# Kernel tuning notes

Measured on AMD Instinct MI355X. Metric: run time of the kernel, lower is better.

## Reference

```python
import jax, jax.numpy as jnp
import numpy as np

N_NODES = 50000
N_REL = 16
N_BASIS = 8
D_IN = 64
D_HID = 64
N_CLASS = 16
N_EDGES = 800000


def setup_inputs() -> dict:
    key = jax.random.key(0)
    ks = jax.random.split(key, 9)
    x = jax.random.normal(ks[0], (N_NODES, D_IN), dtype=jnp.float32)
    edge_index = jax.random.randint(ks[1], (2, N_EDGES), 0, N_NODES, dtype=jnp.int64)
    edge_type = jax.random.randint(ks[2], (N_EDGES,), 0, N_REL, dtype=jnp.int64)
    s1 = 1.0 / np.sqrt(D_IN)
    s2 = 1.0 / np.sqrt(D_HID)
    # layer 1: basis decomposition W_r = sum_b coeffs[r,b] * bases[b]
    bases1 = jax.random.normal(ks[3], (N_BASIS, D_IN, D_HID), dtype=jnp.float32) * s1
    coeffs1 = jax.random.normal(ks[4], (N_REL, N_BASIS), dtype=jnp.float32)
    self1 = jax.random.normal(ks[5], (D_IN, D_HID), dtype=jnp.float32) * s1
    # layer 2
    bases2 = jax.random.normal(ks[6], (N_BASIS, D_HID, N_CLASS), dtype=jnp.float32) * s2
    coeffs2 = jax.random.normal(ks[7], (N_REL, N_BASIS), dtype=jnp.float32)
    self2 = jax.random.normal(ks[8], (D_HID, N_CLASS), dtype=jnp.float32) * s2
    return {"x": x, "bases1": bases1, "coeffs1": coeffs1, "self1": self1,
            "bases2": bases2, "coeffs2": coeffs2, "self2": self2,
            "edge_index": edge_index, "edge_type": edge_type}


def _rgcn_layer(h, bases, coeffs, self_w, src, seg_id, inv_c):
    # normalized messages gathered from source nodes: [E, d]
    msg = h[src] * inv_c[:, None]
    # fused per-(relation, target-node) segment reduce -> [R, N, d]
    agg = jax.ops.segment_sum(msg, seg_id, num_segments=N_REL * N_NODES)
    agg = agg.reshape(N_REL, N_NODES, -1)
    # per-relation weights from basis decomposition: [R, d_in, d_out]
    w_rel = jnp.einsum('rb,bio->rio', coeffs, bases)
    return jnp.einsum('rni,rio->no', agg, w_rel) + h @ self_w


def reference(x, bases1, coeffs1, self1, bases2, coeffs2, self2, edge_index, edge_type):
    src, dst = edge_index[0], edge_index[1]
    # normalization constants: per-relation in-degree of each target node
    counts = jnp.zeros((N_REL, N_NODES), dtype=jnp.float32).at[edge_type, dst].add(1.0)
    inv_c = 1.0 / jnp.maximum(counts[edge_type, dst], 1.0)  # [E]
    seg_id = edge_type * N_NODES + dst  # combined (relation, node) segment key
    h = jax.nn.relu(_rgcn_layer(x, bases1, coeffs1, self1, src, seg_id, inv_c))
    logits = _rgcn_layer(h, bases2, coeffs2, self2, src, seg_id, inv_c)
    return logits
```

## Files before the change

kernel.cpp:

```cpp
#include <hip/hip_runtime.h>

#define N_NODES 50000
#define N_REL 16
#define N_BASIS 8
#define N_EDGES 800000
#define G1_BLOCKS 782
#define SC_BLOCKS 3125
#define WREL_BLOCKS 340
#define ZERO_BLOCKS 49
#define CAP 64

typedef short s8v __attribute__((ext_vector_type(8)));
typedef float f4v __attribute__((ext_vector_type(4)));

__device__ inline unsigned short f2bf(float f) {
    union { float f; unsigned u; } v; v.f = f;
    unsigned r = (v.u + 0x7FFFu + ((v.u >> 16) & 1u)) >> 16;
    return (unsigned short)r;
}
__device__ inline float bf2f(unsigned short b) {
    union { unsigned u; float f; } v; v.u = ((unsigned)b) << 16;
    return v.f;
}
__device__ __forceinline__ void acc8(float* a, float inv, int4 p) {
    a[0] += inv * __int_as_float((int)((unsigned)p.x << 16));
    a[1] += inv * __int_as_float(p.x & (int)0xFFFF0000u);
    a[2] += inv * __int_as_float((int)((unsigned)p.y << 16));
    a[3] += inv * __int_as_float(p.y & (int)0xFFFF0000u);
    a[4] += inv * __int_as_float((int)((unsigned)p.z << 16));
    a[5] += inv * __int_as_float(p.z & (int)0xFFFF0000u);
    a[6] += inv * __int_as_float((int)((unsigned)p.w << 16));
    a[7] += inv * __int_as_float(p.w & (int)0xFFFF0000u);
}

__global__ __launch_bounds__(256) void k_pre(const float* __restrict__ b1, const float* __restrict__ c1,
                                             const float* __restrict__ s1f,
                                             const float* __restrict__ b2, const float* __restrict__ c2,
                                             const float* __restrict__ s2f,
                                             unsigned short* __restrict__ w1T,
                                             unsigned short* __restrict__ w2T,
                                             int* __restrict__ cursor) {
    int bid = blockIdx.x;
    if (bid >= WREL_BLOCKS) {
        int i = (bid - WREL_BLOCKS) * 256 + threadIdx.x;
        if (i < 12504) ((int4*)cursor)[i] = make_int4(0, 0, 0, 0);
        return;
    }
    int idx = bid * 256 + threadIdx.x;
    if (idx < 17 * 4096) {
        int r = idx >> 12, o = (idx >> 6) & 63, k = idx & 63;
        float acc = 0.f;
        if (r < 16) {
            #pragma unroll
            for (int b = 0; b < N_BASIS; b++) acc += c1[r * N_BASIS + b] * b1[b * 4096 + k * 64 + o];
        } else {
            acc = s1f[k * 64 + o];
        }
        w1T[idx] = f2bf(acc);
    } else {
        int idx2 = idx - 17 * 4096;
        if (idx2 < 17 * 1024) {
            int r = idx2 >> 10, o = (idx2 >> 6) & 15, k = idx2 & 63;
            float acc = 0.f;
            if (r < 16) {
                #pragma unroll
                for (int b = 0; b < N_BASIS; b++) acc += c2[r * N_BASIS + b] * b2[b * 1024 + k * 16 + o];
            } else {
                acc = s2f[k * 16 + o];
            }
            w2T[idx2] = f2bf(acc);
        }
    }
}

__device__ __forceinline__ void gemm1_tile(int tile, int tid,
                                           const float* __restrict__ x,
                                           const unsigned short* __restrict__ w1T,
                                           unsigned short* __restrict__ t1,
                                           unsigned short* __restrict__ h,
                                           unsigned short* wbuf,
                                           unsigned short* ou) {
    int wv = tid >> 6, lane = tid & 63;
    int m = lane & 15, q = lane >> 4;
    int nb = tile * 64 + wv * 16;
    bool active = (nb < N_NODES);
    int n = active ? (nb + m) : 0;

    const float* xr = x + (size_t)n * 64 + q * 8;
    float4 x0a = *(const float4*)(xr);
    float4 x0b = *(const float4*)(xr + 4);
    float4 x1a = *(const float4*)(xr + 32);
    float4 x1b = *(const float4*)(xr + 36);
    s8v b0, b1;
    b0[0] = f2bf(x0a.x); b0[1] = f2bf(x0a.y); b0[2] = f2bf(x0a.z); b0[3] = f2bf(x0a.w);
    b0[4] = f2bf(x0b.x); b0[5] = f2bf(x0b.y); b0[6] = f2bf(x0b.z); b0[7] = f2bf(x0b.w);
    b1[0] = f2bf(x1a.x); b1[1] = f2bf(x1a.y); b1[2] = f2bf(x1a.z); b1[3] = f2bf(x1a.w);
    b1[4] = f2bf(x1b.x); b1[5] = f2bf(x1b.y); b1[6] = f2bf(x1b.z); b1[7] = f2bf(x1b.w);

    int c0 = tid, c1 = tid + 256;
    int p0s = (c0 >> 3) * 64 + (((c0 & 7) ^ ((c0 >> 3) & 7)) << 3);
    int p1s = (c1 >> 3) * 64 + (((c1 & 7) ^ ((c1 >> 3) & 7)) << 3);

    {
        const int4* src = (const int4*)w1T;
        int4 v0 = src[c0], v1 = src[c1];
        *(int4*)&wbuf[p0s] = v0;
        *(int4*)&wbuf[p1s] = v1;
    }
    __syncthreads();

    for (int w = 0; w < 17; w++) {
        int cur = w & 1;
        if (w < 16) {
            const int4* src = (const int4*)w1T + (w + 1) * 512;
            int4 v0 = src[c0], v1 = src[c1];
            *(int4*)&wbuf[(cur ^ 1) * 4096 + p0s] = v0;
            *(int4*)&wbuf[(cur ^ 1) * 4096 + p1s] = v1;
        }
        #pragma unroll
        for (int ct = 0; ct < 4; ct++) {
            int ro = ct * 16 + m;
            int pa = q ^ (ro & 7);
            int pb = (4 + q) ^ (ro & 7);
            s8v A0 = *(const s8v*)&wbuf[cur * 4096 + ro * 64 + pa * 8];
            s8v A1 = *(const s8v*)&wbuf[cur * 4096 + ro * 64 + pb * 8];
            f4v acc = (f4v){0.f, 0.f, 0.f, 0.f};
            acc = __builtin_amdgcn_mfma_f32_16x16x32_bf16(A0, b0, acc, 0, 0, 0);
            acc = __builtin_amdgcn_mfma_f32_16x16x32_bf16(A1, b1, acc, 0, 0, 0);
            ushort4 o4;
            o4.x = f2bf(acc[0]); o4.y = f2bf(acc[1]); o4.z = f2bf(acc[2]); o4.w = f2bf(acc[3]);
            int g = ct * 2 + (q >> 1);
            int pg = g ^ (m & 7);
            *(ushort4*)&ou[wv * 1024 + m * 64 + pg * 8 + (q & 1) * 4] = o4;
        }
        if (active) {
            int r1 = lane >> 3, g1 = lane & 7;
            int pg1 = g1 ^ (r1 & 7);
            int4 d0 = *(const int4*)&ou[wv * 1024 + r1 * 64 + pg1 * 8];
            int4 d1 = *(const int4*)&ou[wv * 1024 + (r1 + 8) * 64 + pg1 * 8];
            unsigned short* base = (w < 16) ? (t1 + ((size_t)w * N_NODES + nb) * 64)
                                            : (h + (size_t)nb * 64);
            *(int4*)(base + lane * 8) = d0;
            *(int4*)(base + 512 + lane * 8) = d1;
        }
        __syncthreads();
    }
}

__global__ __launch_bounds__(256) void k_fused1(const float* __restrict__ x,
                                                const unsigned short* __restrict__ w1T,
                                                unsigned short* __restrict__ t1,
                                                unsigned short* __restrict__ h,
                                                const int* __restrict__ ei,
                                                const int* __restrict__ et,
                                                int* __restrict__ cursor,
                                                int* __restrict__ sed) {
    __shared__ __align__(16) unsigned short wbuf[2 * 4096];
    __shared__ __align__(16) unsigned short ou[4 * 1024];
    if (blockIdx.x >= G1_BLOCKS) {
        int e = (blockIdx.x - G1_BLOCKS) * 256 + threadIdx.x;
        if (e < N_EDGES) {
            int src = ei[e];
            int dst = ei[N_EDGES + e];
            int t = et[e];
            int pos = atomicAdd(&cursor[dst], 1);
            if (pos < CAP) sed[dst * CAP + pos] = (t << 16) | src;
        }
        return;
    }
    gemm1_tile(blockIdx.x, threadIdx.x, x, w1T, t1, h, wbuf, ou);
}

__global__ __launch_bounds__(256) void k_aggt(const int* __restrict__ cursor,
                                              const int* __restrict__ sed,
                                              const unsigned short* __restrict__ t1,
                                              const unsigned short* __restrict__ h,
                                              const unsigned short* __restrict__ w2T,
                                              unsigned short* __restrict__ t2,
                                              float* __restrict__ out) {
    __shared__ int hist[16][16];
    __shared__ __align__(16) unsigned short htile[16][72];
    int tid = threadIdx.x;
    int nb = blockIdx.x * 16;
    int j = tid >> 4;
    int sub = tid & 15;
    int n = nb + j;
    int deg = cursor[n];
    deg = deg < CAP ? deg : CAP;
    const int* bucket = sed + n * CAP;

    hist[j][sub] = 0;
    for (int i = sub; i < deg; i += 16)
        atomicAdd(&hist[j][bucket[i] >> 16], 1);

    int slot = sub >> 3;
    int d8 = sub & 7;
    float a[8];
    #pragma unroll
    for (int k = 0; k < 8; k++) a[k] = 0.f;
    for (int i = slot; i < deg; i += 4) {
        int e0 = bucket[i];
        bool has1 = (i + 2) < deg;
        int e1 = has1 ? bucket[i + 2] : e0;
        int t0 = e0 >> 16, s0 = e0 & 0xFFFF;
        int t1i = e1 >> 16, s1 = e1 & 0xFFFF;
        float inv0 = 1.0f / (float)hist[j][t0];
        float inv1 = has1 ? (1.0f / (float)hist[j][t1i]) : 0.f;
        int4 p0 = *(const int4*)(t1 + ((size_t)(t0 * N_NODES + s0)) * 64 + d8 * 8);
        int4 p1 = *(const int4*)(t1 + ((size_t)(t1i * N_NODES + s1)) * 64 + d8 * 8);
        acc8(a, inv0, p0);
        acc8(a, inv1, p1);
    }
    #pragma unroll
    for (int k = 0; k < 8; k++) a[k] += __shfl_xor(a[k], 8, 64);
    if (slot == 0) {
        int4 hs = *(const int4*)(h + (size_t)n * 64 + d8 * 8);
        acc8(a, 1.0f, hs);
        ushort4 lo, hi;
        lo.x = f2bf(a[0] > 0.f ? a[0] : 0.f);
        lo.y = f2bf(a[1] > 0.f ? a[1] : 0.f);
        lo.z = f2bf(a[2] > 0.f ? a[2] : 0.f);
        lo.w = f2bf(a[3] > 0.f ? a[3] : 0.f);
        hi.x = f2bf(a[4] > 0.f ? a[4] : 0.f);
        hi.y = f2bf(a[5] > 0.f ? a[5] : 0.f);
        hi.z = f2bf(a[6] > 0.f ? a[6] : 0.f);
        hi.w = f2bf(a[7] > 0.f ? a[7] : 0.f);
        *(ushort4*)&htile[j][d8 * 8] = lo;
        *(ushort4*)&htile[j][d8 * 8 + 4] = hi;
    }
    __syncthreads();

    int wv = tid >> 6, lane = tid & 63;
    int m = lane & 15, q = lane >> 4;
    int nn = nb + m;
    s8v b0 = *(const s8v*)&htile[m][q * 8];
    s8v b1 = *(const s8v*)&htile[m][32 + q * 8];
    const unsigned short* wp = w2T + m * 64 + q * 8;

    #pragma unroll
    for (int j5 = 0; j5 < 4; j5++) {
        int w = wv * 4 + j5;
        s8v A0 = *(const s8v*)(wp + (w << 10));
        s8v A1 = *(const s8v*)(wp + (w << 10) + 32);
        f4v acc = (f4v){0.f, 0.f, 0.f, 0.f};
        acc = __builtin_amdgcn_mfma_f32_16x16x32_bf16(A0, b0, acc, 0, 0, 0);
        acc = __builtin_amdgcn_mfma_f32_16x16x32_bf16(A1, b1, acc, 0, 0, 0);
        ushort4 o;
        o.x = f2bf(acc[0]); o.y = f2bf(acc[1]); o.z = f2bf(acc[2]); o.w = f2bf(acc[3]);
        *(ushort4*)(t2 + ((size_t)w * N_NODES + nn) * 16 + q * 4) = o;
    }
    if (wv == 0) {
        s8v A0 = *(const s8v*)(wp + (16 << 10));
        s8v A1 = *(const s8v*)(wp + (16 << 10) + 32);
        f4v acc = (f4v){0.f, 0.f, 0.f, 0.f};
        acc = __builtin_amdgcn_mfma_f32_16x16x32_bf16(A0, b0, acc, 0, 0, 0);
        acc = __builtin_amdgcn_mfma_f32_16x16x32_bf16(A1, b1, acc, 0, 0, 0);
        *(float4*)(out + (size_t)nn * 16 + q * 4) = make_float4(acc[0], acc[1], acc[2], acc[3]);
    }
}

__global__ __launch_bounds__(256) void k_agg2(const int* __restrict__ cursor,
                                              const int* __restrict__ sed,
                                              const unsigned short* __restrict__ t2,
                                              float* __restrict__ out) {
    __shared__ int hist[16][16];
    int tid = threadIdx.x;
    int j = tid >> 4;
    int sub = tid & 15;
    int n = blockIdx.x * 16 + j;
    int deg = cursor[n];
    deg = deg < CAP ? deg : CAP;
    const int* bucket = sed + n * CAP;

    hist[j][sub] = 0;
    for (int i = sub; i < deg; i += 16)
        atomicAdd(&hist[j][bucket[i] >> 16], 1);

    int slot = sub >> 1;
    int d2 = sub & 1;
    float a[8];
    #pragma unroll
    for (int k = 0; k < 8; k++) a[k] = 0.f;
    for (int i = slot; i < deg; i += 16) {
        int e0 = bucket[i];
        bool has1 = (i + 8) < deg;
        int e1 = has1 ? bucket[i + 8] : e0;
        int t0 = e0 >> 16, s0 = e0 & 0xFFFF;
        int t1i = e1 >> 16, s1 = e1 & 0xFFFF;
        float inv0 = 1.0f / (float)hist[j][t0];
        float inv1 = has1 ? (1.0f / (float)hist[j][t1i]) : 0.f;
        int4 p0 = *(const int4*)(t2 + ((size_t)(t0 * N_NODES + s0)) * 16 + d2 * 8);
        int4 p1 = *(const int4*)(t2 + ((size_t)(t1i * N_NODES + s1)) * 16 + d2 * 8);
        acc8(a, inv0, p0);
        acc8(a, inv1, p1);
    }
    #pragma unroll
    for (int k = 0; k < 8; k++) {
        a[k] += __shfl_xor(a[k], 2, 64);
        a[k] += __shfl_xor(a[k], 4, 64);
        a[k] += __shfl_xor(a[k], 8, 64);
    }
    if (slot == 0) {
        float* p = out + (size_t)n * 16 + d2 * 8;
        float4 c0 = *(const float4*)p;
        float4 c1 = *(const float4*)(p + 4);
        c0.x += a[0]; c0.y += a[1]; c0.z += a[2]; c0.w += a[3];
        c1.x += a[4]; c1.y += a[5]; c1.z += a[6]; c1.w += a[7];
        *(float4*)p = c0;
        *(float4*)(p + 4) = c1;
    }
}

extern "C" void kernel_launch(void* const* d_in, const int* in_sizes, int n_in,
                              void* d_out, int out_size, void* d_ws, size_t ws_size,
                              hipStream_t stream) {
    const float* x      = (const float*)d_in[0];
    const float* bases1 = (const float*)d_in[1];
    const float* coeffs1= (const float*)d_in[2];
    const float* self1  = (const float*)d_in[3];
    const float* bases2 = (const float*)d_in[4];
    const float* coeffs2= (const float*)d_in[5];
    const float* self2  = (const float*)d_in[6];
    const int*   ei     = (const int*)d_in[7];
    const int*   et     = (const int*)d_in[8];
    float* out = (float*)d_out;

    char* ws = (char*)d_ws;
    int*            cursor = (int*)(ws + 0);
    unsigned short* w1T    = (unsigned short*)(ws + 200064);
    unsigned short* w2T    = (unsigned short*)(ws + 339328);
    int*            sed    = (int*)(ws + 374144);
    unsigned short* h      = (unsigned short*)(ws + 13174144);
    unsigned short* t1     = (unsigned short*)(ws + 19574144);
    unsigned short* t2     = (unsigned short*)(ws + 121974144);

    k_pre<<<WREL_BLOCKS + ZERO_BLOCKS, 256, 0, stream>>>(
        bases1, coeffs1, self1, bases2, coeffs2, self2, w1T, w2T, cursor);
    k_fused1<<<G1_BLOCKS + SC_BLOCKS, 256, 0, stream>>>(x, w1T, t1, h, ei, et, cursor, sed);
    k_aggt<<<SC_BLOCKS, 256, 0, stream>>>(cursor, sed, t1, h, w2T, t2, out);
    k_agg2<<<SC_BLOCKS, 256, 0, stream>>>(cursor, sed, t2, out);
}
```

Measured before the change: 183.4 us.

## Aggregate raw features per relation before transforming instead of pre-transforming all nodes

Drops the old order of transforming every node by all 17 relation weight matrices and then gathering. Each node now first gathers and mean-averages its neighbours' bf16 features per relation in shared memory, after sorting its edges by relation with a histogram and prefix sum. It then applies the relation weights with MFMA over the 16 per-relation aggregates plus the self term. This removes the large t1/t2 intermediates (16×N×64 bf16 for layer one) and their write/read traffic. In exchange the per-node bucket sort costs shared-memory atomics and syncs, the per-relation gather loops are serialized, the second layer's matmul runs on only one wave, and x gets a separate bf16 conversion pass.

Result: slower. 327.0 us (+78.3%).

```diff
diff --git a/kernel.cpp b/kernel.cpp
--- a/kernel.cpp
+++ b/kernel.cpp
@@ -4,11 +4,13 @@
 #define N_REL 16
 #define N_BASIS 8
 #define N_EDGES 800000
-#define G1_BLOCKS 782
-#define SC_BLOCKS 3125
+#define CAP 64
+
 #define WREL_BLOCKS 340
 #define ZERO_BLOCKS 49
-#define CAP 64
+#define XBF_BLOCKS 1563
+#define SC_BLOCKS 3125
+#define AGG_BLOCKS 3125
 
 typedef short s8v __attribute__((ext_vector_type(8)));
 typedef float f4v __attribute__((ext_vector_type(4)));
@@ -18,29 +20,38 @@
     unsigned r = (v.u + 0x7FFFu + ((v.u >> 16) & 1u)) >> 16;
     return (unsigned short)r;
 }
-__device__ inline float bf2f(unsigned short b) {
-    union { unsigned u; float f; } v; v.u = ((unsigned)b) << 16;
-    return v.f;
-}
-__device__ __forceinline__ void acc8(float* a, float inv, int4 p) {
-    a[0] += inv * __int_as_float((int)((unsigned)p.x << 16));
-    a[1] += inv * __int_as_float(p.x & (int)0xFFFF0000u);
-    a[2] += inv * __int_as_float((int)((unsigned)p.y << 16));
-    a[3] += inv * __int_as_float(p.y & (int)0xFFFF0000u);
-    a[4] += inv * __int_as_float((int)((unsigned)p.z << 16));
-    a[5] += inv * __int_as_float(p.z & (int)0xFFFF0000u);
-    a[6] += inv * __int_as_float((int)((unsigned)p.w << 16));
-    a[7] += inv * __int_as_float(p.w & (int)0xFFFF0000u);
-}
-
-__global__ __launch_bounds__(256) void k_pre(const float* __restrict__ b1, const float* __restrict__ c1,
+
+__device__ __forceinline__ void acc4(float* a, int2 p) {
+    a[0] += __int_as_float((int)((unsigned)p.x << 16));
+    a[1] += __int_as_float(p.x & (int)0xFFFF0000u);
+    a[2] += __int_as_float((int)((unsigned)p.y << 16));
+    a[3] += __int_as_float(p.y & (int)0xFFFF0000u);
+}
+
+__global__ __launch_bounds__(256) void k_pre(const float* __restrict__ x,
+                                             const float* __restrict__ b1, const float* __restrict__ c1,
                                              const float* __restrict__ s1f,
                                              const float* __restrict__ b2, const float* __restrict__ c2,
                                              const float* __restrict__ s2f,
                                              unsigned short* __restrict__ w1T,
                                              unsigned short* __restrict__ w2T,
+                                             unsigned short* __restrict__ xbf,
                                              int* __restrict__ cursor) {
     int bid = blockIdx.x;
+    if (bid >= WREL_BLOCKS + ZERO_BLOCKS) {
+        int i = (bid - WREL_BLOCKS - ZERO_BLOCKS) * 256 + threadIdx.x;
+        if (i < 400000) {
+            const float4* xs = (const float4*)x + (size_t)i * 2;
+            float4 v0 = xs[0], v1 = xs[1];
+            int4 w;
+            w.x = (int)(((unsigned)f2bf(v0.y) << 16) | f2bf(v0.x));
+            w.y = (int)(((unsigned)f2bf(v0.w) << 16) | f2bf(v0.z));
+            w.z = (int)(((unsigned)f2bf(v1.y) << 16) | f2bf(v1.x));
+            w.w = (int)(((unsigned)f2bf(v1.w) << 16) | f2bf(v1.z));
+            *(int4*)(xbf + (size_t)i * 8) = w;
+        }
+        return;
+    }
     if (bid >= WREL_BLOCKS) {
         int i = (bid - WREL_BLOCKS) * 256 + threadIdx.x;
         if (i < 12504) ((int4*)cursor)[i] = make_int4(0, 0, 0, 0);
@@ -73,242 +84,162 @@
     }
 }
 
-__device__ __forceinline__ void gemm1_tile(int tile, int tid,
-                                           const float* __restrict__ x,
-                                           const unsigned short* __restrict__ w1T,
-                                           unsigned short* __restrict__ t1,
-                                           unsigned short* __restrict__ h,
-                                           unsigned short* wbuf,
-                                           unsigned short* ou) {
-    int wv = tid >> 6, lane = tid & 63;
-    int m = lane & 15, q = lane >> 4;
-    int nb = tile * 64 + wv * 16;
-    bool active = (nb < N_NODES);
-    int n = active ? (nb + m) : 0;
-
-    const float* xr = x + (size_t)n * 64 + q * 8;
-    float4 x0a = *(const float4*)(xr);
-    float4 x0b = *(const float4*)(xr + 4);
-    float4 x1a = *(const float4*)(xr + 32);
-    float4 x1b = *(const float4*)(xr + 36);
-    s8v b0, b1;
-    b0[0] = f2bf(x0a.x); b0[1] = f2bf(x0a.y); b0[2] = f2bf(x0a.z); b0[3] = f2bf(x0a.w);
-    b0[4] = f2bf(x0b.x); b0[5] = f2bf(x0b.y); b0[6] = f2bf(x0b.z); b0[7] = f2bf(x0b.w);
-    b1[0] = f2bf(x1a.x); b1[1] = f2bf(x1a.y); b1[2] = f2bf(x1a.z); b1[3] = f2bf(x1a.w);
-    b1[4] = f2bf(x1b.x); b1[5] = f2bf(x1b.y); b1[6] = f2bf(x1b.z); b1[7] = f2bf(x1b.w);
-
-    int c0 = tid, c1 = tid + 256;
-    int p0s = (c0 >> 3) * 64 + (((c0 & 7) ^ ((c0 >> 3) & 7)) << 3);
-    int p1s = (c1 >> 3) * 64 + (((c1 & 7) ^ ((c1 >> 3) & 7)) << 3);
-
-    {
-        const int4* src = (const int4*)w1T;
-        int4 v0 = src[c0], v1 = src[c1];
-        *(int4*)&wbuf[p0s] = v0;
-        *(int4*)&wbuf[p1s] = v1;
-    }
+__global__ __launch_bounds__(256) void k_scatter(const int* __restrict__ ei,
+                                                 const int* __restrict__ et,
+                                                 int* __restrict__ cursor,
+                                                 int* __restrict__ sed) {
+    int e = blockIdx.x * 256 + threadIdx.x;
+    if (e < N_EDGES) {
+        int src = ei[e];
+        int dst = ei[N_EDGES + e];
+        int t = et[e];
+        int pos = atomicAdd(&cursor[dst], 1);
+        if (pos < CAP) sed[dst * CAP + pos] = (t << 16) | src;
+    }
+}
+
+#define AGG_PROLOGUE()                                                      \
+    int tid = threadIdx.x;                                                  \
+    int j = tid >> 4, sub = tid & 15;                                       \
+    int nb = blockIdx.x * 16;                                               \
+    int n = nb + j;                                                         \
+    int deg = cursor[n];                                                    \
+    deg = deg < CAP ? deg : CAP;                                            \
+    const int* bucket = sed + n * CAP;                                      \
+    hist[j][sub] = 0;                                                       \
+    __syncthreads();                                                        \
+    for (int i = sub; i < deg; i += 16) {                                   \
+        int e = bucket[i];                                                  \
+        ebr[j][i] = e;                                                      \
+        atomicAdd(&hist[j][e >> 16], 1);                                    \
+    }                                                                       \
+    __syncthreads();                                                        \
+    {                                                                       \
+        int st = 0;                                                         \
+        _Pragma("unroll")                                                   \
+        for (int t = 0; t < 16; t++) { int hv = hist[j][t]; if (t < sub) st += hv; } \
+        sta[j][sub] = st;                                                   \
+        cur[j][sub] = st;                                                   \
+    }                                                                       \
+    __syncthreads();                                                        \
+    for (int i = sub; i < deg; i += 16) {                                   \
+        int e = ebr[j][i];                                                  \
+        int p = atomicAdd(&cur[j][e >> 16], 1);                             \
+        ssrc[j][p] = e & 0xFFFF;                                            \
+    }                                                                       \
     __syncthreads();
 
-    for (int w = 0; w < 17; w++) {
-        int cur = w & 1;
-        if (w < 16) {
-            const int4* src = (const int4*)w1T + (w + 1) * 512;
-            int4 v0 = src[c0], v1 = src[c1];
-            *(int4*)&wbuf[(cur ^ 1) * 4096 + p0s] = v0;
-            *(int4*)&wbuf[(cur ^ 1) * 4096 + p1s] = v1;
-        }
-        #pragma unroll
-        for (int ct = 0; ct < 4; ct++) {
-            int ro = ct * 16 + m;
-            int pa = q ^ (ro & 7);
-            int pb = (4 + q) ^ (ro & 7);
-            s8v A0 = *(const s8v*)&wbuf[cur * 4096 + ro * 64 + pa * 8];
-            s8v A1 = *(const s8v*)&wbuf[cur * 4096 + ro * 64 + pb * 8];
-            f4v acc = (f4v){0.f, 0.f, 0.f, 0.f};
-            acc = __builtin_amdgcn_mfma_f32_16x16x32_bf16(A0, b0, acc, 0, 0, 0);
-            acc = __builtin_amdgcn_mfma_f32_16x16x32_bf16(A1, b1, acc, 0, 0, 0);
-            ushort4 o4;
-            o4.x = f2bf(acc[0]); o4.y = f2bf(acc[1]); o4.z = f2bf(acc[2]); o4.w = f2bf(acc[3]);
-            int g = ct * 2 + (q >> 1);
-            int pg = g ^ (m & 7);
-            *(ushort4*)&ou[wv * 1024 + m * 64 + pg * 8 + (q & 1) * 4] = o4;
-        }
-        if (active) {
-            int r1 = lane >> 3, g1 = lane & 7;
-            int pg1 = g1 ^ (r1 & 7);
-            int4 d0 = *(const int4*)&ou[wv * 1024 + r1 * 64 + pg1 * 8];
-            int4 d1 = *(const int4*)&ou[wv * 1024 + (r1 + 8) * 64 + pg1 * 8];
-            unsigned short* base = (w < 16) ? (t1 + ((size_t)w * N_NODES + nb) * 64)
-                                            : (h + (size_t)nb * 64);
-            *(int4*)(base + lane * 8) = d0;
-            *(int4*)(base + 512 + lane * 8) = d1;
-        }
-        __syncthreads();
-    }
-}
-
-__global__ __launch_bounds__(256) void k_fused1(const float* __restrict__ x,
-                                                const unsigned short* __restrict__ w1T,
-                                                unsigned short* __restrict__ t1,
-                                                unsigned short* __restrict__ h,
-                                                const int* __restrict__ ei,
-                                                const int* __restrict__ et,
-                                                int* __restrict__ cursor,
-                                                int* __restrict__ sed) {
-    __shared__ __align__(16) unsigned short wbuf[2 * 4096];
-    __shared__ __align__(16) unsigned short ou[4 * 1024];
-    if (blockIdx.x >= G1_BLOCKS) {
-        int e = (blockIdx.x - G1_BLOCKS) * 256 + threadIdx.x;
-        if (e < N_EDGES) {
-            int src = ei[e];
-            int dst = ei[N_EDGES + e];
-            int t = et[e];
-            int pos = atomicAdd(&cursor[dst], 1);
-            if (pos < CAP) sed[dst * CAP + pos] = (t << 16) | src;
-        }
-        return;
-    }
-    gemm1_tile(blockIdx.x, threadIdx.x, x, w1T, t1, h, wbuf, ou);
-}
-
-__global__ __launch_bounds__(256) void k_aggt(const int* __restrict__ cursor,
+#define GATHER_ALL(SRCMAT)                                                  \
+    for (int r = 0; r < 16; r++) {                                          \
+        int cnt = hist[j][r];                                               \
+        int s0 = sta[j][r];                                                 \
+        float a[4] = {0.f, 0.f, 0.f, 0.f};                                  \
+        int i = 0;                                                          \
+        for (; i + 2 <= cnt; i += 2) {                                      \
+            int sA = ssrc[j][s0 + i];                                       \
+            int sB = ssrc[j][s0 + i + 1];                                   \
+            int2 pA = *(const int2*)(SRCMAT + sA * 64 + sub * 4);           \
+            int2 pB = *(const int2*)(SRCMAT + sB * 64 + sub * 4);           \
+            acc4(a, pA);                                                    \
+            acc4(a, pB);                                                    \
+        }                                                                   \
+        if (i < cnt) {                                                      \
+            int sA = ssrc[j][s0 + i];                                       \
+            int2 pA = *(const int2*)(SRCMAT + sA * 64 + sub * 4);           \
+            acc4(a, pA);                                                    \
+        }                                                                   \
+        float iv = 1.0f / (float)(cnt > 0 ? cnt : 1);                       \
+        ushort4 o;                                                          \
+        o.x = f2bf(a[0] * iv); o.y = f2bf(a[1] * iv);                       \
+        o.z = f2bf(a[2] * iv); o.w = f2bf(a[3] * iv);                       \
+        *(ushort4*)&agg[r][j][sub * 4] = o;                                 \
+    }                                                                       \
+    __syncthreads();
+
+__global__ __launch_bounds__(256) void k_agg1(const int* __restrict__ cursor,
                                               const int* __restrict__ sed,
-                                              const unsigned short* __restrict__ t1,
-                                              const unsigned short* __restrict__ h,
-                                              const unsigned short* __restrict__ w2T,
-                                              unsigned short* __restrict__ t2,
-                                              float* __restrict__ out) {
+                                              const unsigned short* __restrict__ xbf,
+                                              const unsigned short* __restrict__ w1T,
+                                              unsigned short* __restrict__ h) {
+    __shared__ int ebr[16][64];
+    __shared__ int ssrc[16][64];
     __shared__ int hist[16][16];
-    __shared__ __align__(16) unsigned short htile[16][72];
-    int tid = threadIdx.x;
-    int nb = blockIdx.x * 16;
-    int j = tid >> 4;
-    int sub = tid & 15;
-    int n = nb + j;
-    int deg = cursor[n];
-    deg = deg < CAP ? deg : CAP;
-    const int* bucket = sed + n * CAP;
-
-    hist[j][sub] = 0;
-    for (int i = sub; i < deg; i += 16)
-        atomicAdd(&hist[j][bucket[i] >> 16], 1);
-
-    int slot = sub >> 3;
-    int d8 = sub & 7;
-    float a[8];
-    #pragma unroll
-    for (int k = 0; k < 8; k++) a[k] = 0.f;
-    for (int i = slot; i < deg; i += 4) {
-        int e0 = bucket[i];
-        bool has1 = (i + 2) < deg;
-        int e1 = has1 ? bucket[i + 2] : e0;
-        int t0 = e0 >> 16, s0 = e0 & 0xFFFF;
-        int t1i = e1 >> 16, s1 = e1 & 0xFFFF;
-        float inv0 = 1.0f / (float)hist[j][t0];
-        float inv1 = has1 ? (1.0f / (float)hist[j][t1i]) : 0.f;
-        int4 p0 = *(const int4*)(t1 + ((size_t)(t0 * N_NODES + s0)) * 64 + d8 * 8);
-        int4 p1 = *(const int4*)(t1 + ((size_t)(t1i * N_NODES + s1)) * 64 + d8 * 8);
-        acc8(a, inv0, p0);
-        acc8(a, inv1, p1);
-    }
-    #pragma unroll
-    for (int k = 0; k < 8; k++) a[k] += __shfl_xor(a[k], 8, 64);
-    if (slot == 0) {
-        int4 hs = *(const int4*)(h + (size_t)n * 64 + d8 * 8);
-        acc8(a, 1.0f, hs);
-        ushort4 lo, hi;
-        lo.x = f2bf(a[0] > 0.f ? a[0] : 0.f);
-        lo.y = f2bf(a[1] > 0.f ? a[1] : 0.f);
-        lo.z = f2bf(a[2] > 0.f ? a[2] : 0.f);
-        lo.w = f2bf(a[3] > 0.f ? a[3] : 0.f);
-        hi.x = f2bf(a[4] > 0.f ? a[4] : 0.f);
-        hi.y = f2bf(a[5] > 0.f ? a[5] : 0.f);
-        hi.z = f2bf(a[6] > 0.f ? a[6] : 0.f);
-        hi.w = f2bf(a[7] > 0.f ? a[7] : 0.f);
-        *(ushort4*)&htile[j][d8 * 8] = lo;
-        *(ushort4*)&htile[j][d8 * 8 + 4] = hi;
-    }
-    __syncthreads();
+    __shared__ int cur[16][16];
+    __shared__ int sta[16][16];
+    __shared__ __align__(16) unsigned short agg[16][16][72];
+
+    AGG_PROLOGUE();
+    GATHER_ALL(xbf);
 
     int wv = tid >> 6, lane = tid & 63;
     int m = lane & 15, q = lane >> 4;
     int nn = nb + m;
-    s8v b0 = *(const s8v*)&htile[m][q * 8];
-    s8v b1 = *(const s8v*)&htile[m][32 + q * 8];
-    const unsigned short* wp = w2T + m * 64 + q * 8;
-
-    #pragma unroll
-    for (int j5 = 0; j5 < 4; j5++) {
-        int w = wv * 4 + j5;
-        s8v A0 = *(const s8v*)(wp + (w << 10));
-        s8v A1 = *(const s8v*)(wp + (w << 10) + 32);
-        f4v acc = (f4v){0.f, 0.f, 0.f, 0.f};
-        acc = __builtin_amdgcn_mfma_f32_16x16x32_bf16(A0, b0, acc, 0, 0, 0);
-        acc = __builtin_amdgcn_mfma_f32_16x16x32_bf16(A1, b1, acc, 0, 0, 0);
-        ushort4 o;
-        o.x = f2bf(acc[0]); o.y = f2bf(acc[1]); o.z = f2bf(acc[2]); o.w = f2bf(acc[3]);
-        *(ushort4*)(t2 + ((size_t)w * N_NODES + nn) * 16 + q * 4) = o;
-    }
-    if (wv == 0) {
-        s8v A0 = *(const s8v*)(wp + (16 << 10));
-        s8v A1 = *(const s8v*)(wp + (16 << 10) + 32);
-        f4v acc = (f4v){0.f, 0.f, 0.f, 0.f};
-        acc = __builtin_amdgcn_mfma_f32_16x16x32_bf16(A0, b0, acc, 0, 0, 0);
-        acc = __builtin_amdgcn_mfma_f32_16x16x32_bf16(A1, b1, acc, 0, 0, 0);
-        *(float4*)(out + (size_t)nn * 16 + q * 4) = make_float4(acc[0], acc[1], acc[2], acc[3]);
-    }
+    const unsigned short* wpA = w1T + (wv * 16 + m) * 64 + q * 8;
+    f4v D = (f4v){0.f, 0.f, 0.f, 0.f};
+    #pragma unroll 4
+    for (int r = 0; r < 16; r++) {
+        s8v A0 = *(const s8v*)(wpA + r * 4096);
+        s8v A1 = *(const s8v*)(wpA + r * 4096 + 32);
+        s8v B0 = *(const s8v*)&agg[r][m][q * 8];
+        s8v B1 = *(const s8v*)&agg[r][m][32 + q * 8];
+        D = __builtin_amdgcn_mfma_f32_16x16x32_bf16(A0, B0, D, 0, 0, 0);
+        D = __builtin_amdgcn_mfma_f32_16x16x32_bf16(A1, B1, D, 0, 0, 0);
+    }
+    {
+        s8v A0 = *(const s8v*)(wpA + 16 * 4096);
+        s8v A1 = *(const s8v*)(wpA + 16 * 4096 + 32);
+        s8v B0 = *(const s8v*)(xbf + (size_t)nn * 64 + q * 8);
+        s8v B1 = *(const s8v*)(xbf + (size_t)nn * 64 + 32 + q * 8);
+        D = __builtin_amdgcn_mfma_f32_16x16x32_bf16(A0, B0, D, 0, 0, 0);
+        D = __builtin_amdgcn_mfma_f32_16x16x32_bf16(A1, B1, D, 0, 0, 0);
+    }
+    ushort4 o;
+    o.x = f2bf(D[0] > 0.f ? D[0] : 0.f);
+    o.y = f2bf(D[1] > 0.f ? D[1] : 0.f);
+    o.z = f2bf(D[2] > 0.f ? D[2] : 0.f);
+    o.w = f2bf(D[3] > 0.f ? D[3] : 0.f);
+    *(ushort4*)(h + (size_t)nn * 64 + wv * 16 + q * 4) = o;
 }
 
 __global__ __launch_bounds__(256) void k_agg2(const int* __restrict__ cursor,
                                               const int* __restrict__ sed,
-                                              const unsigned short* __restrict__ t2,
+                                              const unsigned short* __restrict__ h,
+                                              const unsigned short* __restrict__ w2T,
                                               float* __restrict__ out) {
+    __shared__ int ebr[16][64];
+    __shared__ int ssrc[16][64];
     __shared__ int hist[16][16];
-    int tid = threadIdx.x;
-    int j = tid >> 4;
-    int sub = tid & 15;
-    int n = blockIdx.x * 16 + j;
-    int deg = cursor[n];
-    deg = deg < CAP ? deg : CAP;
-    const int* bucket = sed + n * CAP;
-
-    hist[j][sub] = 0;
-    for (int i = sub; i < deg; i += 16)
-        atomicAdd(&hist[j][bucket[i] >> 16], 1);
-
-    int slot = sub >> 1;
-    int d2 = sub & 1;
-    float a[8];
-    #pragma unroll
-    for (int k = 0; k < 8; k++) a[k] = 0.f;
-    for (int i = slot; i < deg; i += 16) {
-        int e0 = bucket[i];
-        bool has1 = (i + 8) < deg;
-        int e1 = has1 ? bucket[i + 8] : e0;
-        int t0 = e0 >> 16, s0 = e0 & 0xFFFF;
-        int t1i = e1 >> 16, s1 = e1 & 0xFFFF;
-        float inv0 = 1.0f / (float)hist[j][t0];
-        float inv1 = has1 ? (1.0f / (float)hist[j][t1i]) : 0.f;
-        int4 p0 = *(const int4*)(t2 + ((size_t)(t0 * N_NODES + s0)) * 16 + d2 * 8);
-        int4 p1 = *(const int4*)(t2 + ((size_t)(t1i * N_NODES + s1)) * 16 + d2 * 8);
-        acc8(a, inv0, p0);
-        acc8(a, inv1, p1);
-    }
-    #pragma unroll
-    for (int k = 0; k < 8; k++) {
-        a[k] += __shfl_xor(a[k], 2, 64);
-        a[k] += __shfl_xor(a[k], 4, 64);
-        a[k] += __shfl_xor(a[k], 8, 64);
-    }
-    if (slot == 0) {
-        float* p = out + (size_t)n * 16 + d2 * 8;
-        float4 c0 = *(const float4*)p;
-        float4 c1 = *(const float4*)(p + 4);
-        c0.x += a[0]; c0.y += a[1]; c0.z += a[2]; c0.w += a[3];
-        c1.x += a[4]; c1.y += a[5]; c1.z += a[6]; c1.w += a[7];
-        *(float4*)p = c0;
-        *(float4*)(p + 4) = c1;
-    }
+    __shared__ int cur[16][16];
+    __shared__ int sta[16][16];
+    __shared__ __align__(16) unsigned short agg[16][16][72];
+
+    AGG_PROLOGUE();
+    GATHER_ALL(h);
+
+    int wv = tid >> 6, lane = tid & 63;
+    if (wv != 0) return;
+    int m = lane & 15, q = lane >> 4;
+    int nn = nb + m;
+    const unsigned short* wpA = w2T + m * 64 + q * 8;
+    f4v D = (f4v){0.f, 0.f, 0.f, 0.f};
+    #pragma unroll 4
+    for (int r = 0; r < 16; r++) {
+        s8v A0 = *(const s8v*)(wpA + r * 1024);
+        s8v A1 = *(const s8v*)(wpA + r * 1024 + 32);
+        s8v B0 = *(const s8v*)&agg[r][m][q * 8];
+        s8v B1 = *(const s8v*)&agg[r][m][32 + q * 8];
+        D = __builtin_amdgcn_mfma_f32_16x16x32_bf16(A0, B0, D, 0, 0, 0);
+        D = __builtin_amdgcn_mfma_f32_16x16x32_bf16(A1, B1, D, 0, 0, 0);
+    }
+    {
+        s8v A0 = *(const s8v*)(wpA + 16 * 1024);
+        s8v A1 = *(const s8v*)(wpA + 16 * 1024 + 32);
+        s8v B0 = *(const s8v*)(h + (size_t)nn * 64 + q * 8);
+        s8v B1 = *(const s8v*)(h + (size_t)nn * 64 + 32 + q * 8);
+        D = __builtin_amdgcn_mfma_f32_16x16x32_bf16(A0, B0, D, 0, 0, 0);
+        D = __builtin_amdgcn_mfma_f32_16x16x32_bf16(A1, B1, D, 0, 0, 0);
+    }
+    *(float4*)(out + (size_t)nn * 16 + q * 4) = make_float4(D[0], D[1], D[2], D[3]);
 }
 
 extern "C" void kernel_launch(void* const* d_in, const int* in_sizes, int n_in,
@@ -330,13 +261,12 @@
     unsigned short* w1T    = (unsigned short*)(ws + 200064);
     unsigned short* w2T    = (unsigned short*)(ws + 339328);
     int*            sed    = (int*)(ws + 374144);
-    unsigned short* h      = (unsigned short*)(ws + 13174144);
-    unsigned short* t1     = (unsigned short*)(ws + 19574144);
-    unsigned short* t2     = (unsigned short*)(ws + 121974144);
-
-    k_pre<<<WREL_BLOCKS + ZERO_BLOCKS, 256, 0, stream>>>(
-        bases1, coeffs1, self1, bases2, coeffs2, self2, w1T, w2T, cursor);
-    k_fused1<<<G1_BLOCKS + SC_BLOCKS, 256, 0, stream>>>(x, w1T, t1, h, ei, et, cursor, sed);
-    k_aggt<<<SC_BLOCKS, 256, 0, stream>>>(cursor, sed, t1, h, w2T, t2, out);
-    k_agg2<<<SC_BLOCKS, 256, 0, stream>>>(cursor, sed, t2, out);
-}
+    unsigned short* xbf    = (unsigned short*)(ws + 13174144);
+    unsigned short* h      = (unsigned short*)(ws + 19574144);
+
+    k_pre<<<WREL_BLOCKS + ZERO_BLOCKS + XBF_BLOCKS, 256, 0, stream>>>(
+        x, bases1, coeffs1, self1, bases2, coeffs2, self2, w1T, w2T, xbf, cursor);
+    k_scatter<<<SC_BLOCKS, 256, 0, stream>>>(ei, et, cursor, sed);
+    k_agg1<<<AGG_BLOCKS, 256, 0, stream>>>(cursor, sed, xbf, w1T, h);
+    k_agg2<<<AGG_BLOCKS, 256, 0, stream>>>(cursor, sed, h, w2T, out);
+}
```
